# Kernel tuning notes

Measured on AMD Instinct MI355X. Metric: run time of the kernel, lower is better.

The kernel has to match this reference:

```python
import jax, jax.numpy as jnp
import numpy as np

GS, SO = 5, 3  # KANLinear grid_size, spline_order (efficient-kan defaults)


def kan_linear(x, base_w, spline_w, spline_scaler):
    """efficient-kan KANLinear: silu(x)@Wb^T + Bspline(x) contracted with scaled spline weights."""
    g = jnp.arange(-SO, GS + SO + 1, dtype=x.dtype) * (2.0 / GS) - 1.0  # uniform grid, len 12
    xe = x[..., None]                                                    # (..., in, 1)
    bases = ((xe >= g[:-1]) & (xe < g[1:])).astype(x.dtype)              # (..., in, 11)
    for k in range(1, SO + 1):  # Cox-de Boor recursion -> (..., in, 8)
        bases = ((xe - g[:-(k + 1)]) / (g[k:-1] - g[:-(k + 1)])) * bases[..., :-1] \
              + ((g[k + 1:] - xe) / (g[k + 1:] - g[1:-k])) * bases[..., 1:]
    out = jax.nn.silu(x) @ base_w.T
    return out + jnp.einsum('...ik,oik->...o', bases, spline_w * spline_scaler[..., None])


def reference(hidden_states, in_bw, in_sw, in_sc, conv_w, conv_b, x_bw, x_sw, x_sc,
              dt_w, dt_bias, A_logs, Ds, out_bw, out_sw, out_sc):
    B, N, L, Dm = hidden_states.shape
    d_inner, _, d_conv = conv_w.shape
    K = dt_bias.shape[0]          # 4 scan directions
    d_state = A_logs.shape[1]
    dt_rank = dt_w.shape[1]

    xz = kan_linear(hidden_states, in_bw, in_sw, in_sc)          # (B,N,L,2*Di)
    x, z = jnp.split(xz, 2, axis=-1)

    # causal depthwise conv1d + SiLU (torch pads both sides then truncates to L == left-pad)
    xc = x.reshape(B * N, L, d_inner).transpose(0, 2, 1)          # (BN,Di,L)
    xc = jax.lax.conv_general_dilated(xc, conv_w, (1,), [(d_conv - 1, 0)],
                                      dimension_numbers=('NCH', 'OIH', 'NCH'),
                                      feature_group_count=d_inner)
    xc = jax.nn.silu(xc + conv_b[None, :, None])
    x = xc.transpose(0, 2, 1).reshape(B, N, L, d_inner)

    xs = jnp.concatenate([x, jnp.flip(x, axis=2)], axis=1)        # (B,4,L,Di): fwd + seq-reversed

    x_dbl = kan_linear(xs, x_bw, x_sw, x_sc)                      # (B,4,L,R+2S)
    dt, Bs, Cs = jnp.split(x_dbl, [dt_rank, dt_rank + d_state], axis=-1)
    dts = dt @ dt_w.T                                             # (B,4,L,Di)
    delta = jax.nn.softplus(dts + dt_bias[None, :, None, :])      # (B,4,L,Di)
    A = -jnp.exp(A_logs).reshape(K, d_inner, d_state)             # (4,Di,S)

    # selective scan over L (serial data-dependent linear recurrence)
    u_t = xs.transpose(2, 0, 1, 3)      # (L,B,4,Di)
    d_t = delta.transpose(2, 0, 1, 3)   # (L,B,4,Di)
    B_t = Bs.transpose(2, 0, 1, 3)      # (L,B,4,S)
    C_t = Cs.transpose(2, 0, 1, 3)      # (L,B,4,S)

    def step(h, inp):
        u_l, dl, b_l, c_l = inp
        h = h * jnp.exp(dl[..., None] * A) + (dl * u_l)[..., None] * b_l[:, :, None, :]
        return h, jnp.einsum('bkdn,bkn->bkd', h, c_l)

    h0 = jnp.zeros((B, K, d_inner, d_state), xs.dtype)
    _, ys = jax.lax.scan(step, h0, (u_t, d_t, B_t, C_t))          # ys: (L,B,4,Di)

    y = ys.transpose(1, 2, 0, 3) + xs * Ds.reshape(K, d_inner)[None, :, None, :]  # (B,4,L,Di)
    y = y[:, :2] + jnp.flip(y[:, 2:4], axis=2)                    # merge forward/backward scans

    out = jnp.concatenate([y, z], axis=-1)                        # (B,2,L,2*Di)
    return kan_linear(out, out_bw, out_sw, out_sc)                # (B,2,L,Dm)


def setup_inputs() -> dict:
    key = jax.random.key(0)
    B, N, L = 2, 2, 1024
    d_model, d_state, d_conv, K = 512, 16, 4, 4
    d_inner = d_model            # expand=1
    dt_rank = 32                 # ceil(512/16)
    ks = jax.random.split(key, 10)

    def lin(k, o, i):
        return jax.random.normal(k, (o, i), jnp.float32) / np.sqrt(i).astype(np.float32)

    def spl(k, o, i):
        return jax.random.normal(k, (o, i, GS + SO), jnp.float32) * 0.05

    dt = jnp.exp(jax.random.uniform(ks[7], (d_inner,), jnp.float32)
                 * (np.log(0.1) - np.log(0.001)) + np.log(0.001))
    dt = jnp.clip(dt, 1e-4, None)
    inv_dt = dt + jnp.log(-jnp.expm1(-dt))

    std = dt_rank ** -0.5
    return {
        'hidden_states': jax.random.normal(ks[0], (B, N, L, d_model), jnp.float32),
        'in_bw': lin(ks[1], 2 * d_inner, d_model),
        'in_sw': spl(ks[2], 2 * d_inner, d_model),
        'in_sc': jnp.ones((2 * d_inner, d_model), jnp.float32),
        'conv_w': jax.random.normal(ks[3], (d_inner, 1, d_conv), jnp.float32) / np.sqrt(d_conv).astype(np.float32),
        'conv_b': jnp.zeros((d_inner,), jnp.float32),
        'x_bw': lin(ks[4], dt_rank + 2 * d_state, d_inner),
        'x_sw': spl(ks[5], dt_rank + 2 * d_state, d_inner),
        'x_sc': jnp.ones((dt_rank + 2 * d_state, d_inner), jnp.float32),
        'dt_w': jax.random.uniform(ks[6], (d_inner, dt_rank), jnp.float32, -std, std),
        'dt_bias': jnp.tile(inv_dt[None], (K, 1)),
        'A_logs': jnp.log(jnp.tile(jnp.arange(1, d_state + 1, dtype=jnp.float32)[None], (K * d_inner, 1))),
        'Ds': jnp.ones((K * d_inner,), jnp.float32),
        'out_bw': lin(ks[8], d_model, 2 * d_inner),
        'out_sw': spl(ks[9], d_model, 2 * d_inner),
        'out_sc': jnp.ones((d_model, 2 * d_inner), jnp.float32),
    }
```

## Files before the change

kernel.cpp:

```cpp
#include <hip/hip_runtime.h>
#include <stdint.h>

#define DEV __device__ __forceinline__

typedef __attribute__((ext_vector_type(8))) short short8;
typedef __attribute__((ext_vector_type(4))) float f32x4;

DEV unsigned short f2bf(float f) {
    union { float f; uint32_t u; } v; v.f = f;
    uint32_t u = v.u;
    return (unsigned short)((u + 0x7fffu + ((u >> 16) & 1u)) >> 16);
}
DEV float silu_f(float x) { return x / (1.0f + __expf(-x)); }
DEV float softplus_f(float x) { return (x > 20.0f) ? x : log1pf(__expf(x)); }

DEV int tokx(int bk, int l) {
    int b = bk >> 2;
    int nn = bk & 1;
    int lf = (bk & 2) ? (1023 - l) : l;
    return (b * 2 + nn) * 1024 + lf;
}

DEV void bspline8(float x, float* bo) {
    float b[11];
#pragma unroll
    for (int j = 0; j < 11; ++j) {
        float gj  = 0.4f * (float)(j - 3) - 1.0f;
        float gj1 = 0.4f * (float)(j - 2) - 1.0f;
        b[j] = (x >= gj && x < gj1) ? 1.0f : 0.0f;
    }
#pragma unroll
    for (int k = 1; k <= 3; ++k) {
        float inv = 1.0f / (0.4f * (float)k);
#pragma unroll
        for (int j = 0; j + k < 11; ++j) {
            float gj  = 0.4f * (float)(j - 3) - 1.0f;
            float gk1 = 0.4f * (float)(j + k - 2) - 1.0f;
            b[j] = ((x - gj) * b[j] + (gk1 - x) * b[j + 1]) * inv;
        }
    }
#pragma unroll
    for (int j = 0; j < 8; ++j) bo[j] = b[j];
}

__global__ __launch_bounds__(256) void zero_kernel(float4* __restrict__ p, int n4) {
    int i = blockIdx.x * 256 + threadIdx.x;
    if (i < n4) p[i] = make_float4(0.f, 0.f, 0.f, 0.f);
}

__global__ __launch_bounds__(256) void add3_kernel(float4* __restrict__ dst,
        const float4* __restrict__ s1, const float4* __restrict__ s2, int n4) {
    int i = blockIdx.x * 256 + threadIdx.x;
    if (i >= n4) return;
    float4 d = dst[i], a = s1[i], b = s2[i];
    d.x += a.x + b.x; d.y += a.y + b.y; d.z += a.z + b.z; d.w += a.w + b.w;
    dst[i] = d;
}

__global__ __launch_bounds__(256) void wc8_kernel(const float* __restrict__ bw,
        const float* __restrict__ sw, const float* __restrict__ sc,
        unsigned short* __restrict__ Wc, int total) {
    int g = (blockIdx.x * 256 + threadIdx.x) * 8;
    if (g >= total) return;
    float bwv[8], scv[8], swv[64];
    *(float4*)&bwv[0] = *(const float4*)&bw[g];
    *(float4*)&bwv[4] = *(const float4*)&bw[g + 4];
    *(float4*)&scv[0] = *(const float4*)&sc[g];
    *(float4*)&scv[4] = *(const float4*)&sc[g + 4];
#pragma unroll
    for (int q = 0; q < 16; ++q) *(float4*)&swv[q * 4] = *(const float4*)&sw[(size_t)g * 8 + q * 4];
    unsigned short buf[72];
#pragma unroll
    for (int e = 0; e < 8; ++e) {
        buf[e * 9] = f2bf(bwv[e]);
#pragma unroll
        for (int j = 0; j < 8; ++j) buf[e * 9 + 1 + j] = f2bf(swv[e * 8 + j] * scv[e]);
    }
    unsigned short* o = Wc + (size_t)g * 9;
#pragma unroll
    for (int q = 0; q < 9; ++q) *(short8*)&o[q * 8] = *(short8*)&buf[q * 8];
}

__global__ __launch_bounds__(256) void feat8_kernel(const float* __restrict__ X,
        unsigned short* __restrict__ F, int total) {
    int g = (blockIdx.x * 256 + threadIdx.x) * 8;
    if (g >= total) return;
    float xv[8];
    *(float4*)&xv[0] = *(const float4*)&X[g];
    *(float4*)&xv[4] = *(const float4*)&X[g + 4];
    unsigned short buf[72];
#pragma unroll
    for (int e = 0; e < 8; ++e) {
        float x = xv[e];
        buf[e * 9] = f2bf(silu_f(x));
        float bo[8];
        bspline8(x, bo);
#pragma unroll
        for (int j = 0; j < 8; ++j) buf[e * 9 + 1 + j] = f2bf(bo[j]);
    }
    unsigned short* o = F + (size_t)g * 9;
#pragma unroll
    for (int q = 0; q < 9; ++q) *(short8*)&o[q * 8] = *(short8*)&buf[q * 8];
}

template<int BM, int BN, int DEPTH, bool ATOMIC>
__global__ __launch_bounds__(256) void gemm_mfma2(const unsigned short* __restrict__ A,
        const unsigned short* __restrict__ B, float* __restrict__ C0,
        float* __restrict__ C1, float* __restrict__ C2,
        int M, int N, int K, int klen, int gx, int gy, int gz) {
    constexpr int NB  = DEPTH + 2;
    constexpr int FRM = BM / 32;
    constexpr int FRN = BN / 32;
    constexpr int GLA = (BM * 64) / 4096;
    constexpr int GLB = (BN * 64) / 4096;
    constexpr int GL  = GLA + GLB;
    constexpr int LDA = BM * 32;
    constexpr int LDB = BN * 32;
    __shared__ unsigned short As[NB * LDA];
    __shared__ unsigned short Bs[NB * LDB];

    const int nwg = gx * gy * gz;
    int fid = (blockIdx.z * gy + blockIdx.y) * gx + blockIdx.x;
    int cpx = nwg >> 3;
    fid = (fid & 7) * cpx + (fid >> 3);
    const int bx = fid % gx;
    const int by = (fid / gx) % gy;
    const int bz = fid / (gx * gy);

    const int tid = threadIdx.x;
    const int lane = tid & 63;
    const int w = tid >> 6;
    const int wr = w >> 1, wc = w & 1;
    const int bm = bx * BM, bn = by * BN;
    const int kbase = bz * klen;
    const int NT = klen / 32;
    const int frow = lane & 15;
    const int uq = ((lane >> 4) ^ ((frow >> 1) & 3)) * 8;

    float* __restrict__ C = (bz == 0) ? C0 : (bz == 1) ? C1 : C2;

    f32x4 acc[FRM][FRN];
#pragma unroll
    for (int m = 0; m < FRM; ++m)
#pragma unroll
        for (int n = 0; n < FRN; ++n)
            acc[m][n] = (f32x4){0.f, 0.f, 0.f, 0.f};

    auto stage = [&](int t, int buf) {
        const int k0 = kbase + t * 32;
#pragma unroll
        for (int r = 0; r < GLA; ++r) {
            int bo = r * 4096 + tid * 16;
            int row = bo >> 6;
            int lu = ((bo >> 4) & 3) ^ ((row >> 1) & 3);
            __builtin_amdgcn_global_load_lds(
                (const __attribute__((address_space(1))) void*)((const char*)A + ((size_t)(bm + row) * K + k0) * 2 + lu * 16),
                (__attribute__((address_space(3))) void*)((char*)As + (size_t)buf * LDA * 2 + bo), 16, 0, 0);
        }
#pragma unroll
        for (int r = 0; r < GLB; ++r) {
            int bo = r * 4096 + tid * 16;
            int row = bo >> 6;
            int lu = ((bo >> 4) & 3) ^ ((row >> 1) & 3);
            __builtin_amdgcn_global_load_lds(
                (const __attribute__((address_space(1))) void*)((const char*)B + ((size_t)(bn + row) * K + k0) * 2 + lu * 16),
                (__attribute__((address_space(3))) void*)((char*)Bs + (size_t)buf * LDB * 2 + bo), 16, 0, 0);
        }
    };

    auto compute = [&](int buf) {
        const unsigned short* as = As + (size_t)buf * LDA;
        const unsigned short* bs = Bs + (size_t)buf * LDB;
        short8 af[FRM], bf[FRN];
#pragma unroll
        for (int m = 0; m < FRM; ++m)
            af[m] = *(const short8*)&as[(wr * (BM / 2) + m * 16 + frow) * 32 + uq];
#pragma unroll
        for (int n = 0; n < FRN; ++n)
            bf[n] = *(const short8*)&bs[(wc * (BN / 2) + n * 16 + frow) * 32 + uq];
#pragma unroll
        for (int m = 0; m < FRM; ++m)
#pragma unroll
            for (int n = 0; n < FRN; ++n)
                acc[m][n] = __builtin_amdgcn_mfma_f32_16x16x32_bf16(af[m], bf[n], acc[m][n], 0, 0, 0);
    };

    for (int t = 0; t < DEPTH; ++t) stage(t, t);

    int rb = 0, sb = DEPTH;
    int t = 0;
    for (; t + DEPTH < NT; ++t) {
        stage(t + DEPTH, sb);
        asm volatile("s_waitcnt vmcnt(%0)" :: "i"(DEPTH * GL) : "memory");
        asm volatile("s_barrier" ::: "memory");
        compute(rb);
        rb = (rb + 1 == NB) ? 0 : rb + 1;
        sb = (sb + 1 == NB) ? 0 : sb + 1;
    }
    for (; t < NT; ++t) {
        asm volatile("s_waitcnt vmcnt(0)" ::: "memory");
        asm volatile("s_barrier" ::: "memory");
        compute(rb);
        rb = (rb + 1 == NB) ? 0 : rb + 1;
    }

    const int crow = (lane >> 4) * 4;
    const int ccol = lane & 15;
#pragma unroll
    for (int m = 0; m < FRM; ++m)
#pragma unroll
        for (int n = 0; n < FRN; ++n) {
            int gr = bm + wr * (BM / 2) + m * 16 + crow;
            int gc = bn + wc * (BN / 2) + n * 16 + ccol;
#pragma unroll
            for (int r = 0; r < 4; ++r) {
                if (ATOMIC) atomicAdd(&C[(size_t)(gr + r) * N + gc], acc[m][n][r]);
                else        C[(size_t)(gr + r) * N + gc] = acc[m][n][r];
            }
        }
}

__global__ __launch_bounds__(256) void conv_xs_kernel(const float* __restrict__ xz,
        const float* __restrict__ cw, const float* __restrict__ cb,
        float* __restrict__ xsb) {
    int idx = blockIdx.x * 256 + threadIdx.x;
    int d = idx & 511;
    int l = (idx >> 9) & 1023;
    int bn = idx >> 19;
    const float* xcol = xz + (size_t)(bn * 1024) * 1024 + d;
    float acc = cb[d];
#pragma unroll
    for (int h = 0; h < 4; ++h) {
        int ls = l - 3 + h;
        float xv = (ls >= 0) ? xcol[(size_t)ls * 1024] : 0.0f;
        acc = fmaf(cw[d * 4 + h], xv, acc);
    }
    xsb[((size_t)bn * 1024 + l) * 512 + d] = silu_f(acc);
}

__global__ __launch_bounds__(256) void dts_kernel(const float* __restrict__ xdbl,
        const float* __restrict__ dtw, float* __restrict__ dts) {
    int t = blockIdx.x >> 1;
    int half = blockIdx.x & 1;
    int d = half * 256 + threadIdx.x;
    __shared__ float dtv[32];
    if (threadIdx.x < 32) dtv[threadIdx.x] = xdbl[(size_t)t * 64 + threadIdx.x];
    __syncthreads();
    const float* w = dtw + (size_t)d * 32;
    float acc = 0.0f;
#pragma unroll
    for (int r = 0; r < 32; r += 4) {
        float4 wv = *(const float4*)(w + r);
        acc = fmaf(dtv[r], wv.x, acc);
        acc = fmaf(dtv[r + 1], wv.y, acc);
        acc = fmaf(dtv[r + 2], wv.z, acc);
        acc = fmaf(dtv[r + 3], wv.w, acc);
    }
    dts[(size_t)t * 512 + d] = acc;
}

__global__ __launch_bounds__(256) void scanA_kernel(const float* __restrict__ dts,
        const float* __restrict__ xsb, const float* __restrict__ xdbl,
        const float* __restrict__ A_logs, const float* __restrict__ dtb,
        float* __restrict__ P, float* __restrict__ Q) {
    int half = blockIdx.x & 1;
    int chunk = (blockIdx.x >> 1) & 31;
    int bk = blockIdx.x >> 6;
    int k = bk & 3;
    int d = half * 256 + threadIdx.x;
    __shared__ float Bl[32][16];
    for (int s = threadIdx.x; s < 32 * 16; s += 256) {
        int ll = s >> 4, n = s & 15;
        Bl[ll][n] = xdbl[(size_t)tokx(bk, chunk * 32 + ll) * 64 + 32 + n];
    }
    __syncthreads();
    float An[16];
#pragma unroll
    for (int n = 0; n < 16; ++n) An[n] = -__expf(A_logs[(size_t)(k * 512 + d) * 16 + n]);
    float bias = dtb[k * 512 + d];
    float h[16] = {};
    float p[16];
#pragma unroll
    for (int n = 0; n < 16; ++n) p[n] = 1.0f;
    for (int ll = 0; ll < 32; ++ll) {
        size_t off = (size_t)tokx(bk, chunk * 32 + ll) * 512 + d;
        float da = softplus_f(dts[off] + bias);
        float du = da * xsb[off];
#pragma unroll
        for (int n = 0; n < 16; ++n) {
            float a = __expf(da * An[n]);
            h[n] = fmaf(h[n], a, du * Bl[ll][n]);
            p[n] *= a;
        }
    }
    size_t pb = ((size_t)(bk * 32 + chunk) * 16) * 512 + d;
#pragma unroll
    for (int n = 0; n < 16; ++n) { P[pb + n * 512] = p[n]; Q[pb + n * 512] = h[n]; }
}

__global__ __launch_bounds__(512) void scanB_kernel(const float* __restrict__ P,
        const float* __restrict__ Q, float* __restrict__ Hst) {
    int bk = blockIdx.x >> 4;
    int n  = blockIdx.x & 15;
    int d  = threadIdx.x;
    float h = 0.0f;
    for (int chunk = 0; chunk < 32; ++chunk) {
        size_t base = ((size_t)((bk * 32 + chunk) * 16 + n)) * 512 + d;
        Hst[base] = h;
        h = fmaf(P[base], h, Q[base]);
    }
}

__global__ __launch_bounds__(256) void scanC_kernel(const float* __restrict__ dts,
        const float* __restrict__ xsb, const float* __restrict__ xdbl,
        const float* __restrict__ A_logs, const float* __restrict__ dtb,
        const float* __restrict__ Hst, const float* __restrict__ Ds,
        float* __restrict__ ys) {
    int half = blockIdx.x & 1;
    int chunk = (blockIdx.x >> 1) & 31;
    int bk = blockIdx.x >> 6;
    int k = bk & 3;
    int d = half * 256 + threadIdx.x;
    __shared__ float BC[32][32];
    for (int s = threadIdx.x; s < 32 * 32; s += 256) {
        int ll = s >> 5, n = s & 31;
        BC[ll][n] = xdbl[(size_t)tokx(bk, chunk * 32 + ll) * 64 + 32 + n];
    }
    __syncthreads();
    float An[16];
#pragma unroll
    for (int n = 0; n < 16; ++n) An[n] = -__expf(A_logs[(size_t)(k * 512 + d) * 16 + n]);
    float bias = dtb[k * 512 + d];
    float h[16];
    size_t hb = ((size_t)(bk * 32 + chunk) * 16) * 512 + d;
#pragma unroll
    for (int n = 0; n < 16; ++n) h[n] = Hst[hb + n * 512];
    float Dv = Ds[k * 512 + d];
    for (int ll = 0; ll < 32; ++ll) {
        int l = chunk * 32 + ll;
        size_t off = (size_t)tokx(bk, l) * 512 + d;
        float da = softplus_f(dts[off] + bias);
        float u = xsb[off];
        float du = da * u;
        float y = 0.0f;
#pragma unroll
        for (int n = 0; n < 16; ++n) {
            float a = __expf(da * An[n]);
            h[n] = fmaf(h[n], a, du * BC[ll][n]);
            y = fmaf(h[n], BC[ll][16 + n], y);
        }
        ys[((size_t)bk * 1024 + l) * 512 + d] = fmaf(u, Dv, y);
    }
}

__global__ __launch_bounds__(256) void merge_kernel(const float* __restrict__ ys,
        float* __restrict__ xz) {
    int idx = blockIdx.x * 256 + threadIdx.x;
    int d = idx & 511;
    int l = (idx >> 9) & 1023;
    int nn = (idx >> 19) & 1;
    int b = idx >> 20;
    float v = ys[((size_t)(b * 4 + nn) * 1024 + l) * 512 + d]
            + ys[((size_t)(b * 4 + nn + 2) * 1024 + (1023 - l)) * 512 + d];
    size_t trow = (size_t)(b * 2 + nn) * 1024 + l;
    xz[trow * 1024 + d] = v;
}

extern "C" void kernel_launch(void* const* d_in, const int* in_sizes, int n_in,
                              void* d_out, int out_size, void* d_ws, size_t ws_size,
                              hipStream_t stream) {
    const float* hidden  = (const float*)d_in[0];
    const float* in_bw   = (const float*)d_in[1];
    const float* in_sw   = (const float*)d_in[2];
    const float* in_sc   = (const float*)d_in[3];
    const float* conv_w  = (const float*)d_in[4];
    const float* conv_b  = (const float*)d_in[5];
    const float* x_bw    = (const float*)d_in[6];
    const float* x_sw    = (const float*)d_in[7];
    const float* x_sc    = (const float*)d_in[8];
    const float* dt_w    = (const float*)d_in[9];
    const float* dt_bias = (const float*)d_in[10];
    const float* A_logs  = (const float*)d_in[11];
    const float* Ds      = (const float*)d_in[12];
    const float* out_bw  = (const float*)d_in[13];
    const float* out_sw  = (const float*)d_in[14];
    const float* out_sc  = (const float*)d_in[15];
    float* out = (float*)d_out;
    char* ws = (char*)d_ws;

    float* XZ    = (float*)(ws + 0);
    float* XSB   = (float*)(ws + 16777216);
    float* XDBL  = (float*)(ws + 25165824);
    float* DTS   = (float*)(ws + 26214400);
    char*  zone  = ws + 34603008;
    unsigned short* FEAT = (unsigned short*)zone;
    float* YS    = (float*)zone;
    float* P     = (float*)(zone + 16777216);
    float* Q     = (float*)(zone + 25165824);
    float* HST   = (float*)(zone + 33554432);
    float* XZP1  = (float*)(zone + 37748736);
    float* XZP2  = (float*)(zone + 54525952);
    float* OP1   = (float*)(ws + 16777216);
    float* OP2   = (float*)(ws + 26214400);
    unsigned short* WCbuf = (unsigned short*)(ws + 110100480);
    unsigned short* WC2   = (unsigned short*)(ws + 119537664);

    wc8_kernel<<<256, 256, 0, stream>>>(in_bw, in_sw, in_sc, WCbuf, 1024 * 512);
    wc8_kernel<<<16, 256, 0, stream>>>(x_bw, x_sw, x_sc, WC2, 64 * 512);

    feat8_kernel<<<1024, 256, 0, stream>>>(hidden, FEAT, 4096 * 512);
    gemm_mfma2<128, 128, 1, false><<<dim3(32, 8, 3), 256, 0, stream>>>(
        FEAT, WCbuf, XZ, XZP1, XZP2, 4096, 1024, 4608, 1536, 32, 8, 3);
    add3_kernel<<<4096, 256, 0, stream>>>((float4*)XZ, (const float4*)XZP1, (const float4*)XZP2, (4096 * 1024) / 4);

    wc8_kernel<<<256, 256, 0, stream>>>(out_bw, out_sw, out_sc, WCbuf, 512 * 1024);

    conv_xs_kernel<<<8192, 256, 0, stream>>>(XZ, conv_w, conv_b, XSB);

    feat8_kernel<<<1024, 256, 0, stream>>>(XSB, FEAT, 4096 * 512);
    zero_kernel<<<256, 256, 0, stream>>>((float4*)XDBL, (4096 * 64) / 4);
    gemm_mfma2<64, 64, 1, true><<<dim3(64, 1, 8), 256, 0, stream>>>(
        FEAT, WC2, XDBL, XDBL, XDBL, 4096, 64, 4608, 576, 64, 1, 8);

    dts_kernel<<<8192, 256, 0, stream>>>(XDBL, dt_w, DTS);

    scanA_kernel<<<512, 256, 0, stream>>>(DTS, XSB, XDBL, A_logs, dt_bias, P, Q);
    scanB_kernel<<<128, 512, 0, stream>>>(P, Q, HST);
    scanC_kernel<<<512, 256, 0, stream>>>(DTS, XSB, XDBL, A_logs, dt_bias, HST, Ds, YS);

    merge_kernel<<<8192, 256, 0, stream>>>(YS, XZ);

    feat8_kernel<<<2048, 256, 0, stream>>>(XZ, FEAT, 4096 * 1024);
    gemm_mfma2<128, 64, 1, false><<<dim3(32, 8, 3), 256, 0, stream>>>(
        FEAT, WCbuf, out, OP1, OP2, 4096, 512, 9216, 3072, 32, 8, 3);
    add3_kernel<<<2048, 256, 0, stream>>>((float4*)out, (const float4*)OP1, (const float4*)OP2, (4096 * 512) / 4);
}
```

Baseline: 486.8 us.

## Drop multi-buffered LDS pipeline in GEMM, use single buffer and 4-way split-K

```diff
diff --git a/kernel.cpp b/kernel.cpp
--- a/kernel.cpp
+++ b/kernel.cpp
@@ -54,6 +54,17 @@
     if (i >= n4) return;
     float4 d = dst[i], a = s1[i], b = s2[i];
     d.x += a.x + b.x; d.y += a.y + b.y; d.z += a.z + b.z; d.w += a.w + b.w;
+    dst[i] = d;
+}
+
+__global__ __launch_bounds__(256) void add4_kernel(float4* __restrict__ dst,
+        const float4* __restrict__ s1, const float4* __restrict__ s2,
+        const float4* __restrict__ s3, int n4) {
+    int i = blockIdx.x * 256 + threadIdx.x;
+    if (i >= n4) return;
+    float4 d = dst[i], a = s1[i], b = s2[i], c = s3[i];
+    d.x += a.x + b.x + c.x; d.y += a.y + b.y + c.y;
+    d.z += a.z + b.z + c.z; d.w += a.w + b.w + c.w;
     dst[i] = d;
 }
 
@@ -103,21 +114,17 @@
     for (int q = 0; q < 9; ++q) *(short8*)&o[q * 8] = *(short8*)&buf[q * 8];
 }
 
-template<int BM, int BN, int DEPTH, bool ATOMIC>
-__global__ __launch_bounds__(256) void gemm_mfma2(const unsigned short* __restrict__ A,
+template<int BM, int BN, bool ATOMIC>
+__global__ __launch_bounds__(256) void gemm_mfma3(const unsigned short* __restrict__ A,
         const unsigned short* __restrict__ B, float* __restrict__ C0,
-        float* __restrict__ C1, float* __restrict__ C2,
+        float* __restrict__ C1, float* __restrict__ C2, float* __restrict__ C3,
         int M, int N, int K, int klen, int gx, int gy, int gz) {
-    constexpr int NB  = DEPTH + 2;
     constexpr int FRM = BM / 32;
     constexpr int FRN = BN / 32;
     constexpr int GLA = (BM * 64) / 4096;
     constexpr int GLB = (BN * 64) / 4096;
-    constexpr int GL  = GLA + GLB;
-    constexpr int LDA = BM * 32;
-    constexpr int LDB = BN * 32;
-    __shared__ unsigned short As[NB * LDA];
-    __shared__ unsigned short Bs[NB * LDB];
+    __shared__ unsigned short As[BM * 32];
+    __shared__ unsigned short Bs[BN * 32];
 
     const int nwg = gx * gy * gz;
     int fid = (blockIdx.z * gy + blockIdx.y) * gx + blockIdx.x;
@@ -137,7 +144,7 @@
     const int frow = lane & 15;
     const int uq = ((lane >> 4) ^ ((frow >> 1) & 3)) * 8;
 
-    float* __restrict__ C = (bz == 0) ? C0 : (bz == 1) ? C1 : C2;
+    float* __restrict__ C = (bz == 0) ? C0 : (bz == 1) ? C1 : (bz == 2) ? C2 : C3;
 
     f32x4 acc[FRM][FRN];
 #pragma unroll
@@ -146,7 +153,7 @@
         for (int n = 0; n < FRN; ++n)
             acc[m][n] = (f32x4){0.f, 0.f, 0.f, 0.f};
 
-    auto stage = [&](int t, int buf) {
+    for (int t = 0; t < NT; ++t) {
         const int k0 = kbase + t * 32;
 #pragma unroll
         for (int r = 0; r < GLA; ++r) {
@@ -155,7 +162,7 @@
             int lu = ((bo >> 4) & 3) ^ ((row >> 1) & 3);
             __builtin_amdgcn_global_load_lds(
                 (const __attribute__((address_space(1))) void*)((const char*)A + ((size_t)(bm + row) * K + k0) * 2 + lu * 16),
-                (__attribute__((address_space(3))) void*)((char*)As + (size_t)buf * LDA * 2 + bo), 16, 0, 0);
+                (__attribute__((address_space(3))) void*)((char*)As + bo), 16, 0, 0);
         }
 #pragma unroll
         for (int r = 0; r < GLB; ++r) {
@@ -164,44 +171,23 @@
             int lu = ((bo >> 4) & 3) ^ ((row >> 1) & 3);
             __builtin_amdgcn_global_load_lds(
                 (const __attribute__((address_space(1))) void*)((const char*)B + ((size_t)(bn + row) * K + k0) * 2 + lu * 16),
-                (__attribute__((address_space(3))) void*)((char*)Bs + (size_t)buf * LDB * 2 + bo), 16, 0, 0);
-        }
-    };
-
-    auto compute = [&](int buf) {
-        const unsigned short* as = As + (size_t)buf * LDA;
-        const unsigned short* bs = Bs + (size_t)buf * LDB;
+                (__attribute__((address_space(3))) void*)((char*)Bs + bo), 16, 0, 0);
+        }
+        __syncthreads();
+
         short8 af[FRM], bf[FRN];
 #pragma unroll
         for (int m = 0; m < FRM; ++m)
-            af[m] = *(const short8*)&as[(wr * (BM / 2) + m * 16 + frow) * 32 + uq];
+            af[m] = *(const short8*)&As[(wr * (BM / 2) + m * 16 + frow) * 32 + uq];
 #pragma unroll
         for (int n = 0; n < FRN; ++n)
-            bf[n] = *(const short8*)&bs[(wc * (BN / 2) + n * 16 + frow) * 32 + uq];
+            bf[n] = *(const short8*)&Bs[(wc * (BN / 2) + n * 16 + frow) * 32 + uq];
 #pragma unroll
         for (int m = 0; m < FRM; ++m)
 #pragma unroll
             for (int n = 0; n < FRN; ++n)
                 acc[m][n] = __builtin_amdgcn_mfma_f32_16x16x32_bf16(af[m], bf[n], acc[m][n], 0, 0, 0);
-    };
-
-    for (int t = 0; t < DEPTH; ++t) stage(t, t);
-
-    int rb = 0, sb = DEPTH;
-    int t = 0;
-    for (; t + DEPTH < NT; ++t) {
-        stage(t + DEPTH, sb);
-        asm volatile("s_waitcnt vmcnt(%0)" :: "i"(DEPTH * GL) : "memory");
-        asm volatile("s_barrier" ::: "memory");
-        compute(rb);
-        rb = (rb + 1 == NB) ? 0 : rb + 1;
-        sb = (sb + 1 == NB) ? 0 : sb + 1;
-    }
-    for (; t < NT; ++t) {
-        asm volatile("s_waitcnt vmcnt(0)" ::: "memory");
-        asm volatile("s_barrier" ::: "memory");
-        compute(rb);
-        rb = (rb + 1 == NB) ? 0 : rb + 1;
+        __syncthreads();
     }
 
     const int crow = (lane >> 4) * 4;
@@ -400,6 +386,7 @@
     float* HST   = (float*)(zone + 33554432);
     float* XZP1  = (float*)(zone + 37748736);
     float* XZP2  = (float*)(zone + 54525952);
+    float* XZP3  = (float*)(ws + 16777216);
     float* OP1   = (float*)(ws + 16777216);
     float* OP2   = (float*)(ws + 26214400);
     unsigned short* WCbuf = (unsigned short*)(ws + 110100480);
@@ -409,9 +396,10 @@
     wc8_kernel<<<16, 256, 0, stream>>>(x_bw, x_sw, x_sc, WC2, 64 * 512);
 
     feat8_kernel<<<1024, 256, 0, stream>>>(hidden, FEAT, 4096 * 512);
-    gemm_mfma2<128, 128, 1, false><<<dim3(32, 8, 3), 256, 0, stream>>>(
-        FEAT, WCbuf, XZ, XZP1, XZP2, 4096, 1024, 4608, 1536, 32, 8, 3);
-    add3_kernel<<<4096, 256, 0, stream>>>((float4*)XZ, (const float4*)XZP1, (const float4*)XZP2, (4096 * 1024) / 4);
+    gemm_mfma3<128, 128, false><<<dim3(32, 8, 4), 256, 0, stream>>>(
+        FEAT, WCbuf, XZ, XZP1, XZP2, XZP3, 4096, 1024, 4608, 1152, 32, 8, 4);
+    add4_kernel<<<4096, 256, 0, stream>>>((float4*)XZ, (const float4*)XZP1,
+        (const float4*)XZP2, (const float4*)XZP3, (4096 * 1024) / 4);
 
     wc8_kernel<<<256, 256, 0, stream>>>(out_bw, out_sw, out_sc, WCbuf, 512 * 1024);
 
@@ -419,8 +407,8 @@
 
     feat8_kernel<<<1024, 256, 0, stream>>>(XSB, FEAT, 4096 * 512);
     zero_kernel<<<256, 256, 0, stream>>>((float4*)XDBL, (4096 * 64) / 4);
-    gemm_mfma2<64, 64, 1, true><<<dim3(64, 1, 8), 256, 0, stream>>>(
-        FEAT, WC2, XDBL, XDBL, XDBL, 4096, 64, 4608, 576, 64, 1, 8);
+    gemm_mfma3<64, 64, true><<<dim3(64, 1, 8), 256, 0, stream>>>(
+        FEAT, WC2, XDBL, XDBL, XDBL, XDBL, 4096, 64, 4608, 576, 64, 1, 8);
 
     dts_kernel<<<8192, 256, 0, stream>>>(XDBL, dt_w, DTS);
 
@@ -431,7 +419,8 @@
     merge_kernel<<<8192, 256, 0, stream>>>(YS, XZ);
 
     feat8_kernel<<<2048, 256, 0, stream>>>(XZ, FEAT, 4096 * 1024);
-    gemm_mfma2<128, 64, 1, false><<<dim3(32, 8, 3), 256, 0, stream>>>(
-        FEAT, WCbuf, out, OP1, OP2, 4096, 512, 9216, 3072, 32, 8, 3);
-    add3_kernel<<<2048, 256, 0, stream>>>((float4*)out, (const float4*)OP1, (const float4*)OP2, (4096 * 512) / 4);
-}
+    gemm_mfma3<128, 64, false><<<dim3(32, 8, 3), 256, 0, stream>>>(
+        FEAT, WCbuf, out, OP1, OP2, OP2, 4096, 512, 9216, 3072, 32, 8, 3);
+    add3_kernel<<<2048, 256, 0, stream>>>((float4*)out, (const float4*)OP1,
+        (const float4*)OP2, (4096 * 512) / 4);
+}
```

Measured after the change: 504.5 us. 3.6% more time.

## Switch KAN feature and weight packing to feature-major layout, reorder GEMM tile mapping

Applied to the files above, without the earlier changes.

```diff
diff --git a/kernel.cpp b/kernel.cpp
--- a/kernel.cpp
+++ b/kernel.cpp
@@ -57,50 +57,63 @@
     dst[i] = d;
 }
 
-__global__ __launch_bounds__(256) void wc8_kernel(const float* __restrict__ bw,
+__global__ __launch_bounds__(256) void wcFM_kernel(const float* __restrict__ bw,
         const float* __restrict__ sw, const float* __restrict__ sc,
-        unsigned short* __restrict__ Wc, int total) {
-    int g = (blockIdx.x * 256 + threadIdx.x) * 8;
-    if (g >= total) return;
+        unsigned short* __restrict__ Wc, int OUT, int IN) {
+    int gid = blockIdx.x * 256 + threadIdx.x;
+    int perRow = IN >> 3;
+    if (gid >= OUT * perRow) return;
+    int o  = gid / perRow;
+    int i0 = (gid % perRow) * 8;
+    const float* bwp = bw + (size_t)o * IN + i0;
+    const float* scp = sc + (size_t)o * IN + i0;
+    const float* swp = sw + ((size_t)o * IN + i0) * 8;
     float bwv[8], scv[8], swv[64];
-    *(float4*)&bwv[0] = *(const float4*)&bw[g];
-    *(float4*)&bwv[4] = *(const float4*)&bw[g + 4];
-    *(float4*)&scv[0] = *(const float4*)&sc[g];
-    *(float4*)&scv[4] = *(const float4*)&sc[g + 4];
-#pragma unroll
-    for (int q = 0; q < 16; ++q) *(float4*)&swv[q * 4] = *(const float4*)&sw[(size_t)g * 8 + q * 4];
-    unsigned short buf[72];
+    *(float4*)&bwv[0] = *(const float4*)bwp;
+    *(float4*)&bwv[4] = *(const float4*)(bwp + 4);
+    *(float4*)&scv[0] = *(const float4*)scp;
+    *(float4*)&scv[4] = *(const float4*)(scp + 4);
+#pragma unroll
+    for (int q = 0; q < 16; ++q) *(float4*)&swv[q * 4] = *(const float4*)(swp + q * 4);
+    unsigned short* row = Wc + (size_t)o * 9 * IN + i0;
+    short8 v;
+#pragma unroll
+    for (int e = 0; e < 8; ++e) v[e] = f2bf(bwv[e]);
+    *(short8*)row = v;
+#pragma unroll
+    for (int j = 1; j <= 8; ++j) {
+#pragma unroll
+        for (int e = 0; e < 8; ++e) v[e] = f2bf(swv[e * 8 + (j - 1)] * scv[e]);
+        *(short8*)&row[(size_t)j * IN] = v;
+    }
+}
+
+__global__ __launch_bounds__(256) void featFM_kernel(const float* __restrict__ X,
+        unsigned short* __restrict__ F, int ntok, int IN) {
+    int gid = blockIdx.x * 256 + threadIdx.x;
+    int perRow = IN >> 3;
+    if (gid >= ntok * perRow) return;
+    int t  = gid / perRow;
+    int i0 = (gid % perRow) * 8;
+    const float* xp = X + (size_t)t * IN + i0;
+    float xv[8];
+    *(float4*)&xv[0] = *(const float4*)xp;
+    *(float4*)&xv[4] = *(const float4*)(xp + 4);
+    float bases[8][8];
+    short8 v;
 #pragma unroll
     for (int e = 0; e < 8; ++e) {
-        buf[e * 9] = f2bf(bwv[e]);
-#pragma unroll
-        for (int j = 0; j < 8; ++j) buf[e * 9 + 1 + j] = f2bf(swv[e * 8 + j] * scv[e]);
-    }
-    unsigned short* o = Wc + (size_t)g * 9;
-#pragma unroll
-    for (int q = 0; q < 9; ++q) *(short8*)&o[q * 8] = *(short8*)&buf[q * 8];
-}
-
-__global__ __launch_bounds__(256) void feat8_kernel(const float* __restrict__ X,
-        unsigned short* __restrict__ F, int total) {
-    int g = (blockIdx.x * 256 + threadIdx.x) * 8;
-    if (g >= total) return;
-    float xv[8];
-    *(float4*)&xv[0] = *(const float4*)&X[g];
-    *(float4*)&xv[4] = *(const float4*)&X[g + 4];
-    unsigned short buf[72];
-#pragma unroll
-    for (int e = 0; e < 8; ++e) {
-        float x = xv[e];
-        buf[e * 9] = f2bf(silu_f(x));
-        float bo[8];
-        bspline8(x, bo);
-#pragma unroll
-        for (int j = 0; j < 8; ++j) buf[e * 9 + 1 + j] = f2bf(bo[j]);
-    }
-    unsigned short* o = F + (size_t)g * 9;
-#pragma unroll
-    for (int q = 0; q < 9; ++q) *(short8*)&o[q * 8] = *(short8*)&buf[q * 8];
+        v[e] = f2bf(silu_f(xv[e]));
+        bspline8(xv[e], bases[e]);
+    }
+    unsigned short* row = F + (size_t)t * 9 * IN + i0;
+    *(short8*)row = v;
+#pragma unroll
+    for (int j = 1; j <= 8; ++j) {
+#pragma unroll
+        for (int e = 0; e < 8; ++e) v[e] = f2bf(bases[e][j - 1]);
+        *(short8*)&row[(size_t)j * IN] = v;
+    }
 }
 
 template<int BM, int BN, int DEPTH, bool ATOMIC>
@@ -123,9 +136,9 @@
     int fid = (blockIdx.z * gy + blockIdx.y) * gx + blockIdx.x;
     int cpx = nwg >> 3;
     fid = (fid & 7) * cpx + (fid >> 3);
-    const int bx = fid % gx;
-    const int by = (fid / gx) % gy;
-    const int bz = fid / (gx * gy);
+    const int by = fid % gy;
+    const int bx = (fid / gy) % gx;
+    const int bz = fid / (gy * gx);
 
     const int tid = threadIdx.x;
     const int lane = tid & 63;
@@ -405,19 +418,19 @@
     unsigned short* WCbuf = (unsigned short*)(ws + 110100480);
     unsigned short* WC2   = (unsigned short*)(ws + 119537664);
 
-    wc8_kernel<<<256, 256, 0, stream>>>(in_bw, in_sw, in_sc, WCbuf, 1024 * 512);
-    wc8_kernel<<<16, 256, 0, stream>>>(x_bw, x_sw, x_sc, WC2, 64 * 512);
-
-    feat8_kernel<<<1024, 256, 0, stream>>>(hidden, FEAT, 4096 * 512);
+    wcFM_kernel<<<256, 256, 0, stream>>>(in_bw, in_sw, in_sc, WCbuf, 1024, 512);
+    wcFM_kernel<<<16, 256, 0, stream>>>(x_bw, x_sw, x_sc, WC2, 64, 512);
+
+    featFM_kernel<<<1024, 256, 0, stream>>>(hidden, FEAT, 4096, 512);
     gemm_mfma2<128, 128, 1, false><<<dim3(32, 8, 3), 256, 0, stream>>>(
         FEAT, WCbuf, XZ, XZP1, XZP2, 4096, 1024, 4608, 1536, 32, 8, 3);
     add3_kernel<<<4096, 256, 0, stream>>>((float4*)XZ, (const float4*)XZP1, (const float4*)XZP2, (4096 * 1024) / 4);
 
-    wc8_kernel<<<256, 256, 0, stream>>>(out_bw, out_sw, out_sc, WCbuf, 512 * 1024);
+    wcFM_kernel<<<256, 256, 0, stream>>>(out_bw, out_sw, out_sc, WCbuf, 512, 1024);
 
     conv_xs_kernel<<<8192, 256, 0, stream>>>(XZ, conv_w, conv_b, XSB);
 
-    feat8_kernel<<<1024, 256, 0, stream>>>(XSB, FEAT, 4096 * 512);
+    featFM_kernel<<<1024, 256, 0, stream>>>(XSB, FEAT, 4096, 512);
     zero_kernel<<<256, 256, 0, stream>>>((float4*)XDBL, (4096 * 64) / 4);
     gemm_mfma2<64, 64, 1, true><<<dim3(64, 1, 8), 256, 0, stream>>>(
         FEAT, WC2, XDBL, XDBL, XDBL, 4096, 64, 4608, 576, 64, 1, 8);
@@ -430,8 +443,9 @@
 
     merge_kernel<<<8192, 256, 0, stream>>>(YS, XZ);
 
-    feat8_kernel<<<2048, 256, 0, stream>>>(XZ, FEAT, 4096 * 1024);
+    featFM_kernel<<<2048, 256, 0, stream>>>(XZ, FEAT, 4096, 1024);
     gemm_mfma2<128, 64, 1, false><<<dim3(32, 8, 3), 256, 0, stream>>>(
         FEAT, WCbuf, out, OP1, OP2, 4096, 512, 9216, 3072, 32, 8, 3);
-    add3_kernel<<<2048, 256, 0, stream>>>((float4*)out, (const float4*)OP1, (const float4*)OP2, (4096 * 512) / 4);
-}
+    add3_kernel<<<2048, 256, 0, stream>>>((float4*)out, (const float4*)OP1,
+        (const float4*)OP2, (4096 * 512) / 4);
+}
```

After: 441.0 us. 1.1x faster.
